# Performance work log

Hardware: AMD Instinct MI355X
Metric: run time of the kernel (lower is better)

The kernel has to match this reference:

```python
import jax, jax.numpy as jnp
import numpy as np

N_EMBED = 1024
NUM_EXPERTS = 8
TOP_K = 2
D_FF = 4 * N_EMBED
B, S = 4, 2048


def setup_inputs() -> dict:
    key = jax.random.key(0)
    ks = jax.random.split(key, 8)
    s = 0.02
    return {
        "x": jax.random.normal(ks[0], (B, S, N_EMBED), jnp.float32),
        "noise": jax.random.normal(ks[1], (B, S, NUM_EXPERTS), jnp.float32),
        "w_route": jax.random.normal(ks[2], (N_EMBED, NUM_EXPERTS), jnp.float32) * s,
        "b_route": jnp.zeros((NUM_EXPERTS,), jnp.float32),
        "w_noise": jax.random.normal(ks[3], (N_EMBED, NUM_EXPERTS), jnp.float32) * s,
        "b_noise": jnp.zeros((NUM_EXPERTS,), jnp.float32),
        "w1": jax.random.normal(ks[4], (NUM_EXPERTS, N_EMBED, D_FF), jnp.float32) * s,
        "b1": jnp.zeros((NUM_EXPERTS, D_FF), jnp.float32),
        "w2": jax.random.normal(ks[5], (NUM_EXPERTS, D_FF, N_EMBED), jnp.float32) * s,
        "b2": jnp.zeros((NUM_EXPERTS, N_EMBED), jnp.float32),
    }


def reference(x, noise, w_route, b_route, w_noise, b_noise, w1, b1, w2, b2):
    # NoisyTopkRouter: logits + N(0,1)*softplus(noise_logits), top-k, softmax
    # over a sparse (-inf filled) logit matrix -> gates are exactly 0 for
    # non-selected experts.
    logits = x @ w_route + b_route                                   # [B,S,E]
    noise_logits = x @ w_noise + b_noise                             # [B,S,E]
    noisy = logits + noise * jax.nn.softplus(noise_logits)           # [B,S,E]
    _, topi = jax.lax.top_k(noisy, TOP_K)                            # [B,S,k]
    sel = jax.nn.one_hot(topi, NUM_EXPERTS, dtype=bool).any(-2)      # [B,S,E]
    sparse_logits = jnp.where(sel, noisy, -jnp.inf)
    gates = jax.nn.softmax(sparse_logits, axis=-1)                   # [B,S,E]

    T = x.shape[0] * x.shape[1]
    xf = x.reshape(T, N_EMBED)                                       # [T,d]
    gf = gates.reshape(T, NUM_EXPERTS)                               # [T,E]

    # Dense per-expert MLP weighted by gates; gate==0 for unselected tokens,
    # so this matches the masked gather/scatter of the original exactly.
    out = jnp.zeros_like(xf)
    for e in range(NUM_EXPERTS):
        h = jax.nn.relu(xf @ w1[e] + b1[e])                          # [T,4d]
        y = h @ w2[e] + b2[e]                                        # [T,d]
        out = out + y * gf[:, e:e + 1]
    return out.reshape(x.shape)
```

## Files before the change

### kernel.cpp

```cpp
#include <hip/hip_runtime.h>

typedef __bf16 bf16_t;
typedef __bf16 bf16x8 __attribute__((ext_vector_type(8)));
typedef __bf16 bf16x4 __attribute__((ext_vector_type(4)));
typedef __bf16 bf16x2 __attribute__((ext_vector_type(2)));
typedef float  f32x4  __attribute__((ext_vector_type(4)));
typedef unsigned int u32;
typedef u32 u32x4 __attribute__((ext_vector_type(4)));

#define T_TOK 8192
#define DIM   1024
#define DFF   4096
#define NEXP  8

__device__ __forceinline__ void gll16(const void* g, void* l) {
    __builtin_amdgcn_global_load_lds(
        (const __attribute__((address_space(1))) char*)g,
        (__attribute__((address_space(3))) char*)l, 16, 0, 0);
}

__device__ __forceinline__ void transpose_tile(
    const float* __restrict__ src, bf16_t* __restrict__ dst,
    int R, int C, int r0, int c0, int tid, u32* lds)
{
    {
        int cg = tid & 15, rp = tid >> 4;
#pragma unroll
        for (int i = 0; i < 2; ++i) {
            int p = rp + i * 16;
            f32x4 a = *(const f32x4*)&src[(size_t)(r0 + 2 * p) * C + c0 + cg * 4];
            f32x4 b = *(const f32x4*)&src[(size_t)(r0 + 2 * p + 1) * C + c0 + cg * 4];
#pragma unroll
            for (int j = 0; j < 4; ++j) {
                int c = cg * 4 + j;
                union { bf16x2 h; u32 w; } cv;
                cv.h[0] = (bf16_t)a[j];
                cv.h[1] = (bf16_t)b[j];
                int ps = p ^ (((c >> 2) & 7) << 2);
                lds[c * 32 + ps] = cv.w;
            }
        }
    }
    __syncthreads();
    {
        int q = tid & 7, ccb = tid >> 3;
#pragma unroll
        for (int i = 0; i < 2; ++i) {
            int cc = ccb + i * 32;
            int ps = (q * 4) ^ ((((cc) >> 2) & 7) << 2);
            u32x4 v = *(const u32x4*)&lds[cc * 32 + ps];
            *(u32x4*)&dst[(size_t)(c0 + cc) * R + r0 + q * 8] = v;
        }
    }
}

__global__ __launch_bounds__(256) void fused_pre_kernel(
    const float* __restrict__ x, const float* __restrict__ noise,
    const float* __restrict__ w_route, const float* __restrict__ b_route,
    const float* __restrict__ w_noise, const float* __restrict__ b_noise,
    const float* __restrict__ w1,
    bf16_t* __restrict__ w1t, bf16_t* __restrict__ xb,
    int* __restrict__ counts, int* __restrict__ lists, float* __restrict__ gate_tok,
    int* __restrict__ inv)
{
    __shared__ u32 lds[64 * 32];
    int id = blockIdx.x;
    int tid = threadIdx.x;

    if (id >= 4096) {
        int t1 = id - 4096;
        int e = t1 >> 10, rem = t1 & 1023;
        int bx = rem & 63, by = rem >> 6;
        transpose_tile(w1 + (size_t)e * DIM * DFF, w1t + (size_t)e * DIM * DFF,
                       DIM, DFF, by * 64, bx * 64, tid, lds);
        return;
    }

    int wave = tid >> 6;
    int lane = tid & 63;

    if (id >= 2048) {
        int tok = (id - 2048) * 4 + wave;
        const f32x4* src = (const f32x4*)(x + (size_t)tok * DIM);
        bf16x8* dst = (bf16x8*)(xb + (size_t)tok * DIM);
#pragma unroll
        for (int j = 0; j < 2; ++j) {
            int c = lane + j * 64;
            f32x4 a = src[c * 2 + 0];
            f32x4 b = src[c * 2 + 1];
            bf16x8 o;
            o[0] = (bf16_t)a[0]; o[1] = (bf16_t)a[1]; o[2] = (bf16_t)a[2]; o[3] = (bf16_t)a[3];
            o[4] = (bf16_t)b[0]; o[5] = (bf16_t)b[1]; o[6] = (bf16_t)b[2]; o[7] = (bf16_t)b[3];
            dst[c] = o;
        }
        return;
    }

    int tok = id * 4 + wave;
    if (tok >= T_TOK) return;

    const float* xr = x + (size_t)tok * DIM;
    double aR[NEXP], aN[NEXP];
#pragma unroll
    for (int e = 0; e < NEXP; ++e) { aR[e] = 0.0; aN[e] = 0.0; }

#pragma unroll 4
    for (int i = 0; i < 16; ++i) {
        int k = lane + i * 64;
        double xv = (double)xr[k];
        const float4* wr4 = (const float4*)(w_route + (size_t)k * 8);
        const float4* wn4 = (const float4*)(w_noise + (size_t)k * 8);
        float4 r0 = wr4[0], r1 = wr4[1];
        float4 n0 = wn4[0], n1 = wn4[1];
        aR[0] += xv * (double)r0.x; aR[1] += xv * (double)r0.y;
        aR[2] += xv * (double)r0.z; aR[3] += xv * (double)r0.w;
        aR[4] += xv * (double)r1.x; aR[5] += xv * (double)r1.y;
        aR[6] += xv * (double)r1.z; aR[7] += xv * (double)r1.w;
        aN[0] += xv * (double)n0.x; aN[1] += xv * (double)n0.y;
        aN[2] += xv * (double)n0.z; aN[3] += xv * (double)n0.w;
        aN[4] += xv * (double)n1.x; aN[5] += xv * (double)n1.y;
        aN[6] += xv * (double)n1.z; aN[7] += xv * (double)n1.w;
    }
#pragma unroll
    for (int e = 0; e < NEXP; ++e) {
        for (int s = 1; s < 64; s <<= 1) {
            aR[e] += __shfl_xor(aR[e], s);
            aN[e] += __shfl_xor(aN[e], s);
        }
    }
    if (lane == 0) {
        double nv[NEXP];
#pragma unroll
        for (int e = 0; e < NEXP; ++e) {
            double lg = aR[e] + (double)b_route[e];
            double nl = aN[e] + (double)b_noise[e];
            double sp = (nl > 30.0) ? nl : log1p(exp(nl));
            nv[e] = lg + (double)noise[(size_t)tok * 8 + e] * sp;
        }
        int i1 = 0;
#pragma unroll
        for (int e = 1; e < NEXP; ++e) if (nv[e] > nv[i1]) i1 = e;
        int i2 = (i1 == 0) ? 1 : 0;
#pragma unroll
        for (int e = 0; e < NEXP; ++e) if (e != i1 && nv[e] > nv[i2]) i2 = e;
        double m = nv[i1];
        double e2 = exp(nv[i2] - m);
        double s = 1.0 + e2;
        gate_tok[2 * tok + 0] = (float)(1.0 / s);
        gate_tok[2 * tok + 1] = (float)(e2 / s);
        int p1 = atomicAdd(&counts[i1], 1);
        lists[i1 * T_TOK + p1] = 2 * tok + 0;
        inv[2 * tok + 0] = (i1 << 13) | p1;
        int p2 = atomicAdd(&counts[i2], 1);
        lists[i2 * T_TOK + p2] = 2 * tok + 1;
        inv[2 * tok + 1] = (i2 << 13) | p2;
    }
}

template<int K, int MODE>
__global__ __launch_bounds__(256) void moe_gemm_kernel(
    const bf16_t* __restrict__ Asrc, const bf16_t* __restrict__ Wt,
    const float* __restrict__ bias,
    const int* __restrict__ counts, const int* __restrict__ lists,
    const float* __restrict__ gate_tok,
    bf16_t* __restrict__ Hout, bf16_t* __restrict__ Yp,
    const float* __restrict__ w2src, bf16_t* __restrict__ w2t)
{
    constexpr int N = (MODE == 0) ? DFF : DIM;
    constexpr int NT = K / 64;
    constexpr int NY = N / 128;

    __shared__ __attribute__((aligned(16))) bf16_t Ah0[128 * 64];
    __shared__ __attribute__((aligned(16))) bf16_t Bh0[128 * 64];
    __shared__ __attribute__((aligned(16))) bf16_t Ah1[128 * 64];
    __shared__ __attribute__((aligned(16))) bf16_t Bh1[128 * 64];

    int wg;
    if constexpr (MODE == 0) {
        wg = blockIdx.x;
        if (wg >= 16384) {
            int t2 = wg - 16384;
            int e = t2 >> 10, rem = t2 & 1023;
            int bx = rem & 15, by = rem >> 4;
            transpose_tile(w2src + (size_t)e * DFF * DIM, w2t + (size_t)e * DFF * DIM,
                           DFF, DIM, by * 64, bx * 64, threadIdx.x, (u32*)Ah0);
            return;
        }
    } else {
        wg = blockIdx.x + 64 * (blockIdx.y + NY * blockIdx.z);
    }

    int e = wg & 7;
    int inner = wg >> 3;
    int xi, yi;
    if constexpr (MODE == 0) {
        int st = inner >> 6, s = inner & 63;
        xi = (st & 7) * 8 + (s & 7);
        yi = (st >> 3) * 8 + (s >> 3);
    } else {
        xi = inner & 63;
        yi = inner >> 6;
    }

    int cnt, base;
    {
        int s = 0, c = 0, b = 0;
#pragma unroll
        for (int i = 0; i < NEXP; ++i) {
            int ci = counts[i];
            if (i == e) { b = s; c = ci; }
            s += ci;
        }
        cnt = c; base = b;
    }
    int m0 = xi * 128;
    if (m0 >= cnt) return;
    int n0 = yi * 128;
    const int* list = lists + e * T_TOK;
    const bf16_t* W = Wt + (size_t)e * N * K;

    int tid = threadIdx.x;
    int lane = tid & 63;
    int wave = tid >> 6;
    int wr = wave >> 1, wc = wave & 1;

    int kcs = (((lane & 7) ^ (lane >> 3)) << 3);
    const bf16_t* pA[4];
    const bf16_t* pB[4];
#pragma unroll
    for (int i = 0; i < 4; ++i) {
        int c = wave * 4 + i;
        int r = c * 8 + (lane >> 3);
        int ridx = m0 + r; if (ridx > cnt - 1) ridx = cnt - 1;
        size_t arow;
        if constexpr (MODE == 0) arow = (size_t)(list[ridx] >> 1);
        else                     arow = (size_t)(base + ridx);
        pA[i] = Asrc + arow * K + kcs;
        pB[i] = W + (size_t)(n0 + r) * K + kcs;
    }

    f32x4 acc[4][4];
#pragma unroll
    for (int m = 0; m < 4; ++m)
#pragma unroll
        for (int n = 0; n < 4; ++n)
            acc[m][n] = (f32x4){0.f, 0.f, 0.f, 0.f};

    int g = lane >> 4, ln15 = lane & 15, ln7 = lane & 7;

#define STAGE(An, Bn, k0) do {                                               \
    _Pragma("unroll") for (int i = 0; i < 4; ++i) {                          \
        int c = wave * 4 + i;                                                \
        gll16(pA[i] + (k0), (An) + c * 512);                                 \
        gll16(pB[i] + (k0), (Bn) + c * 512);                                 \
    } } while (0)

#define COMPUTE(Ab, Bb) do {                                                 \
    _Pragma("unroll") for (int kk = 0; kk < 2; ++kk) {                       \
        bf16x8 a[4], b[4];                                                   \
        int sw = (((kk * 4 + g) ^ ln7) << 3);                                \
        _Pragma("unroll") for (int n = 0; n < 4; ++n)                        \
            b[n] = *(const bf16x8*)((Bb) + (wc * 64 + n * 16 + ln15) * 64 + sw); \
        _Pragma("unroll") for (int m = 0; m < 4; ++m)                        \
            a[m] = *(const bf16x8*)((Ab) + (wr * 64 + m * 16 + ln15) * 64 + sw); \
        __builtin_amdgcn_s_setprio(1);                                       \
        _Pragma("unroll") for (int m = 0; m < 4; ++m)                        \
            _Pragma("unroll") for (int n = 0; n < 4; ++n)                    \
                acc[m][n] = __builtin_amdgcn_mfma_f32_16x16x32_bf16(a[m], b[n], acc[m][n], 0, 0, 0); \
        __builtin_amdgcn_s_setprio(0);                                       \
    } } while (0)

#define FENCE() __builtin_amdgcn_sched_barrier(0)
#define WAITV(n) asm volatile("s_waitcnt vmcnt(" #n ")" ::: "memory")

    STAGE(Ah0, Bh0, 0);

    for (int kt = 0; kt < NT; kt += 2) {
        if (kt + 1 < NT) { STAGE(Ah1, Bh1, (kt + 1) * 64); WAITV(8); }
        else             { WAITV(0); }
        FENCE(); __builtin_amdgcn_s_barrier(); FENCE();
        COMPUTE(Ah0, Bh0);
        FENCE(); __builtin_amdgcn_s_barrier(); FENCE();
        if (kt + 2 < NT) { STAGE(Ah0, Bh0, (kt + 2) * 64); WAITV(8); }
        else             { WAITV(0); }
        FENCE(); __builtin_amdgcn_s_barrier(); FENCE();
        COMPUTE(Ah1, Bh1);
        FENCE(); __builtin_amdgcn_s_barrier(); FENCE();
    }
#undef STAGE
#undef COMPUTE
#undef FENCE
#undef WAITV

    int l4 = lane >> 4;
    float bs[4];
#pragma unroll
    for (int n = 0; n < 4; ++n)
        bs[n] = bias[e * N + n0 + wc * 64 + n * 16 + ln15];
#pragma unroll
    for (int m = 0; m < 4; ++m) {
#pragma unroll
        for (int j = 0; j < 4; ++j) {
            int grow = m0 + wr * 64 + m * 16 + l4 * 4 + j;
            if (grow >= cnt) continue;
            if constexpr (MODE == 0) {
#pragma unroll
                for (int n = 0; n < 4; ++n) {
                    int gcol = n0 + wc * 64 + n * 16 + ln15;
                    float v = acc[m][n][j] + bs[n];
                    Hout[(size_t)(base + grow) * DFF + gcol] = (bf16_t)fmaxf(v, 0.f);
                }
            } else {
                float gt = gate_tok[list[grow]];
#pragma unroll
                for (int n = 0; n < 4; ++n) {
                    int gcol = n0 + wc * 64 + n * 16 + ln15;
                    Yp[(size_t)(base + grow) * DIM + gcol] = (bf16_t)(gt * (acc[m][n][j] + bs[n]));
                }
            }
        }
    }
}

__global__ __launch_bounds__(256) void combine_kernel(
    const bf16_t* __restrict__ Yp, const int* __restrict__ inv,
    const int* __restrict__ counts, float* __restrict__ out)
{
    int bs[NEXP];
    {
        int s = 0;
#pragma unroll
        for (int i = 0; i < NEXP; ++i) { bs[i] = s; s += counts[i]; }
    }
    int q = threadIdx.x >> 7, i = threadIdx.x & 127;
    int t = blockIdx.x * 2 + q;
    int v0 = inv[2 * t], v1 = inv[2 * t + 1];
    int p0 = bs[v0 >> 13] + (v0 & 8191);
    int p1 = bs[v1 >> 13] + (v1 & 8191);
    bf16x8 va = ((const bf16x8*)(Yp + (size_t)p0 * DIM))[i];
    bf16x8 vb = ((const bf16x8*)(Yp + (size_t)p1 * DIM))[i];
    f32x4 o0, o1;
#pragma unroll
    for (int j = 0; j < 4; ++j) {
        o0[j] = (float)va[j] + (float)vb[j];
        o1[j] = (float)va[4 + j] + (float)vb[4 + j];
    }
    f32x4* o = (f32x4*)(out + (size_t)t * DIM + i * 8);
    o[0] = o0;
    o[1] = o1;
}

extern "C" void kernel_launch(void* const* d_in, const int* in_sizes, int n_in,
                              void* d_out, int out_size, void* d_ws, size_t ws_size,
                              hipStream_t stream) {
    const float* x       = (const float*)d_in[0];
    const float* noise   = (const float*)d_in[1];
    const float* w_route = (const float*)d_in[2];
    const float* b_route = (const float*)d_in[3];
    const float* w_noise = (const float*)d_in[4];
    const float* b_noise = (const float*)d_in[5];
    const float* w1      = (const float*)d_in[6];
    const float* b1      = (const float*)d_in[7];
    const float* w2      = (const float*)d_in[8];
    const float* b2      = (const float*)d_in[9];
    float* out = (float*)d_out;

    char* ws = (char*)d_ws;
    size_t off = 0;
    auto alloc = [&](size_t bytes) {
        off = (off + 255) & ~(size_t)255;
        size_t r = off; off += bytes; return r;
    };
    int*    counts   = (int*)   (ws + alloc(32));
    int*    lists    = (int*)   (ws + alloc((size_t)NEXP * T_TOK * 4));
    float*  gate_tok = (float*) (ws + alloc((size_t)T_TOK * 2 * 4));
    int*    inv      = (int*)   (ws + alloc((size_t)T_TOK * 2 * 4));
    bf16_t* w1t      = (bf16_t*)(ws + alloc((size_t)NEXP * DFF * DIM * 2));
    bf16_t* w2t      = (bf16_t*)(ws + alloc((size_t)NEXP * DIM * DFF * 2));
    bf16_t* xb       = (bf16_t*)(ws + alloc((size_t)T_TOK * DIM * 2));
    bf16_t* H        = (bf16_t*)(ws + alloc((size_t)T_TOK * 2 * DFF * 2));
    bf16_t* Yp       = w1t;
    (void)ws_size; (void)in_sizes; (void)n_in; (void)out_size;

    hipMemsetAsync(counts, 0, 32, stream);

    fused_pre_kernel<<<12288, 256, 0, stream>>>(x, noise, w_route, b_route, w_noise, b_noise,
                                                w1, w1t, xb, counts, lists, gate_tok, inv);

    moe_gemm_kernel<DIM, 0><<<24576, 256, 0, stream>>>(
        xb, w1t, b1, counts, lists, gate_tok, H, nullptr, w2, w2t);
    moe_gemm_kernel<DFF, 1><<<dim3(64, DIM / 128, NEXP), 256, 0, stream>>>(
        H, w2t, b2, counts, lists, gate_tok, nullptr, Yp, nullptr, nullptr);

    combine_kernel<<<T_TOK / 2, 256, 0, stream>>>(Yp, inv, counts, out);
}
```

Baseline: 693.1 us.

## Fuse MoE combine into second GEMM epilogue via float atomicAdd on output

Drops the separate combine kernel, the bf16 Yp staging buffer and the inverse index map. The second expert GEMM now scatters gate-weighted results straight into the fp32 output with atomicAdd, after a memset zeroes it. This removes one launch and one round trip through an intermediate buffer, but adds a full-output memset and many scalar, uncoalesced-per-lane float atomics. With only two contributions per element, atomic ordering can also make the output nondeterministic.

```diff
diff --git a/kernel.cpp b/kernel.cpp
--- a/kernel.cpp
+++ b/kernel.cpp
@@ -60,8 +60,7 @@
     const float* __restrict__ w_noise, const float* __restrict__ b_noise,
     const float* __restrict__ w1,
     bf16_t* __restrict__ w1t, bf16_t* __restrict__ xb,
-    int* __restrict__ counts, int* __restrict__ lists, float* __restrict__ gate_tok,
-    int* __restrict__ inv)
+    int* __restrict__ counts, int* __restrict__ lists, float* __restrict__ gate_tok)
 {
     __shared__ u32 lds[64 * 32];
     int id = blockIdx.x;
@@ -150,10 +149,8 @@
         gate_tok[2 * tok + 1] = (float)(e2 / s);
         int p1 = atomicAdd(&counts[i1], 1);
         lists[i1 * T_TOK + p1] = 2 * tok + 0;
-        inv[2 * tok + 0] = (i1 << 13) | p1;
         int p2 = atomicAdd(&counts[i2], 1);
         lists[i2 * T_TOK + p2] = 2 * tok + 1;
-        inv[2 * tok + 1] = (i2 << 13) | p2;
     }
 }
 
@@ -163,7 +160,7 @@
     const float* __restrict__ bias,
     const int* __restrict__ counts, const int* __restrict__ lists,
     const float* __restrict__ gate_tok,
-    bf16_t* __restrict__ Hout, bf16_t* __restrict__ Yp,
+    bf16_t* __restrict__ Hout, float* __restrict__ outp,
     const float* __restrict__ w2src, bf16_t* __restrict__ w2t)
 {
     constexpr int N = (MODE == 0) ? DFF : DIM;
@@ -311,43 +308,17 @@
                     Hout[(size_t)(base + grow) * DFF + gcol] = (bf16_t)fmaxf(v, 0.f);
                 }
             } else {
-                float gt = gate_tok[list[grow]];
+                int entry = list[grow];
+                float gt = gate_tok[entry];
+                float* orow = outp + (size_t)(entry >> 1) * DIM;
 #pragma unroll
                 for (int n = 0; n < 4; ++n) {
                     int gcol = n0 + wc * 64 + n * 16 + ln15;
-                    Yp[(size_t)(base + grow) * DIM + gcol] = (bf16_t)(gt * (acc[m][n][j] + bs[n]));
+                    atomicAdd(&orow[gcol], gt * (acc[m][n][j] + bs[n]));
                 }
             }
         }
     }
-}
-
-__global__ __launch_bounds__(256) void combine_kernel(
-    const bf16_t* __restrict__ Yp, const int* __restrict__ inv,
-    const int* __restrict__ counts, float* __restrict__ out)
-{
-    int bs[NEXP];
-    {
-        int s = 0;
-#pragma unroll
-        for (int i = 0; i < NEXP; ++i) { bs[i] = s; s += counts[i]; }
-    }
-    int q = threadIdx.x >> 7, i = threadIdx.x & 127;
-    int t = blockIdx.x * 2 + q;
-    int v0 = inv[2 * t], v1 = inv[2 * t + 1];
-    int p0 = bs[v0 >> 13] + (v0 & 8191);
-    int p1 = bs[v1 >> 13] + (v1 & 8191);
-    bf16x8 va = ((const bf16x8*)(Yp + (size_t)p0 * DIM))[i];
-    bf16x8 vb = ((const bf16x8*)(Yp + (size_t)p1 * DIM))[i];
-    f32x4 o0, o1;
-#pragma unroll
-    for (int j = 0; j < 4; ++j) {
-        o0[j] = (float)va[j] + (float)vb[j];
-        o1[j] = (float)va[4 + j] + (float)vb[4 + j];
-    }
-    f32x4* o = (f32x4*)(out + (size_t)t * DIM + i * 8);
-    o[0] = o0;
-    o[1] = o1;
 }
 
 extern "C" void kernel_launch(void* const* d_in, const int* in_sizes, int n_in,
@@ -374,23 +345,20 @@
     int*    counts   = (int*)   (ws + alloc(32));
     int*    lists    = (int*)   (ws + alloc((size_t)NEXP * T_TOK * 4));
     float*  gate_tok = (float*) (ws + alloc((size_t)T_TOK * 2 * 4));
-    int*    inv      = (int*)   (ws + alloc((size_t)T_TOK * 2 * 4));
     bf16_t* w1t      = (bf16_t*)(ws + alloc((size_t)NEXP * DFF * DIM * 2));
     bf16_t* w2t      = (bf16_t*)(ws + alloc((size_t)NEXP * DIM * DFF * 2));
     bf16_t* xb       = (bf16_t*)(ws + alloc((size_t)T_TOK * DIM * 2));
     bf16_t* H        = (bf16_t*)(ws + alloc((size_t)T_TOK * 2 * DFF * 2));
-    bf16_t* Yp       = w1t;
     (void)ws_size; (void)in_sizes; (void)n_in; (void)out_size;
 
     hipMemsetAsync(counts, 0, 32, stream);
+    hipMemsetAsync(out, 0, (size_t)T_TOK * DIM * 4, stream);
 
     fused_pre_kernel<<<12288, 256, 0, stream>>>(x, noise, w_route, b_route, w_noise, b_noise,
-                                                w1, w1t, xb, counts, lists, gate_tok, inv);
+                                                w1, w1t, xb, counts, lists, gate_tok);
 
     moe_gemm_kernel<DIM, 0><<<24576, 256, 0, stream>>>(
         xb, w1t, b1, counts, lists, gate_tok, H, nullptr, w2, w2t);
     moe_gemm_kernel<DFF, 1><<<dim3(64, DIM / 128, NEXP), 256, 0, stream>>>(
-        H, w2t, b2, counts, lists, gate_tok, nullptr, Yp, nullptr, nullptr);
-
-    combine_kernel<<<T_TOK / 2, 256, 0, stream>>>(Yp, inv, counts, out);
-}
+        H, w2t, b2, counts, lists, gate_tok, nullptr, out, nullptr, nullptr);
+}
```

Result: slower. 725.1 us (+4.6%).
